# Optimization experiments

Measured on AMD Instinct MI355X. Metric: run time of the kernel, lower is better.

## Reference

```python
import jax, jax.numpy as jnp
import numpy as np

B, T, C, K = 16, 4096, 64, 1024  # K = codebook rows including pad row 0


def setup_inputs() -> dict:
    key = jax.random.key(0)
    k1, k2, k3 = jax.random.split(key, 3)
    z = jax.random.normal(k1, (B, T, C), dtype=jnp.float32)
    codebook_weight = jax.random.normal(k2, (K, C), dtype=jnp.float32)
    # contiguous valid prefixes of random length (torch loop breaks at first 0)
    lengths = jax.random.randint(k3, (B,), T // 2, T + 1)
    mask = (jnp.arange(T)[None, :] < lengths[:, None]).astype(jnp.float32)[:, :, None]
    return {"z": z, "codebook_weight": codebook_weight, "mask": mask}


def _forward(z, codebook_weight, mask):
    # F.normalize(z, p=2, dim=-1) with eps clamp
    z = z / jnp.clip(jnp.linalg.norm(z, axis=-1, keepdims=True), 1e-12)
    e = jax.lax.stop_gradient(codebook_weight)[1:]  # (K-1, C), detached like torch
    zf = z.reshape(-1, C)                            # (B*T, C)
    # squared euclidean distances: ||z||^2 + ||e||^2 - 2 z e^T
    d = (zf * zf).sum(1, keepdims=True) + (e * e).sum(1)[None, :] - 2.0 * (zf @ e.T)
    idx = jnp.argmin(d, axis=1).reshape(B, T)        # (B, T) codes in [0, K-2]
    # scatter(one-hot) @ e  ==  gather rows of e
    z_q = e[idx] * mask                              # (B, T, C)

    valid_count = mask.sum()
    commitment_loss = (jnp.square(z - jax.lax.stop_gradient(z_q)) * mask).sum() / valid_count

    # straight-through estimator
    z_q = z + z_q - jax.lax.stop_gradient(z)

    m1 = mask[:, 1:, :]
    smoothness_loss = (jnp.square(z_q[:, :-1, :] - z_q[:, 1:, :]) * m1).sum() / m1.sum()

    # --- parallel RLE (replaces the host-side python loop) ---
    # torch loop breaks at first mask==0 -> only contiguous valid prefix matters
    mvalid = jnp.cumprod(mask[..., 0], axis=1) > 0   # (B, T) bool
    change = idx[:, 1:] != idx[:, :-1]
    # position 0 always starts a segment; new segment where code changes inside valid prefix
    is_start = jnp.concatenate(
        [jnp.ones((B, 1), dtype=bool), change & mvalid[:, 1:]], axis=1)  # (B, T)
    # stable argsort puts start positions first, in increasing time order
    order = jnp.argsort(jnp.where(is_start, 0, 1), axis=1)               # (B, T)
    n = is_start.sum(axis=1)                                             # segments per batch
    sel_mask = jnp.arange(T)[None, :] < n[:, None]                        # (B, T)
    sel_pos = jnp.where(sel_mask, order, 0)                               # padded to T
    n_mask = sel_mask.astype(jnp.float32)[..., None]                      # (B, T, 1)
    n_z_q = jnp.take_along_axis(z_q, sel_pos[:, :, None], axis=1) * n_mask
    selected_encodings = jnp.where(
        sel_mask, jnp.take_along_axis(idx, sel_pos, axis=1) + 1, 0)       # (B, T) int
    return smoothness_loss, commitment_loss, z_q, n_z_q, n_mask, selected_encodings


def reference(z, codebook_weight, mask):
    return _forward(z, codebook_weight, mask)
```

## Files before the change

### kernel.cpp

```cpp
#include <hip/hip_runtime.h>
#include <math.h>

typedef __attribute__((ext_vector_type(8))) short short8;
typedef __attribute__((ext_vector_type(4))) float f32x4;

#define B_  16
#define T_  4096
#define C_  64
#define KE_ 1023
#define BT_ (B_ * T_)
#define WINHALF 5e-4f


__device__ __forceinline__ unsigned short f2bf(float x) {
    unsigned int u = __float_as_uint(x);
    unsigned int r = (u + 0x7FFFu + ((u >> 16) & 1u)) >> 16;
    return (unsigned short)r;
}
__device__ __forceinline__ float bf2f(unsigned short h) {
    return __uint_as_float(((unsigned int)h) << 16);
}

typedef __attribute__((address_space(1))) const unsigned int g_u32;
typedef __attribute__((address_space(3))) unsigned int l_u32;
__device__ __forceinline__ void gload16(const void* g, void* l) {
    __builtin_amdgcn_global_load_lds((g_u32*)g, (l_u32*)l, 16, 0, 0);
}

__global__ __launch_bounds__(64) void k_prep(const float* __restrict__ cb,
                                             float* __restrict__ ee,
                                             float* __restrict__ ee2,
                                             unsigned short* __restrict__ Eh,
                                             unsigned short* __restrict__ El,
                                             int* __restrict__ flagcnt) {
    const int k = blockIdx.x * 64 + threadIdx.x;
    if (k == 0) *flagcnt = 0;
    unsigned int* EhU = (unsigned int*)Eh;
    unsigned int* ElU = (unsigned int*)El;
    if (k < KE_) {
        const float* r = cb + (size_t)(k + 1) * C_;
        float s = 0.f;
        #pragma unroll
        for (int c = 0; c < C_; c += 2) {
            const float x0 = r[c], x1 = r[c + 1];
            s = fmaf(x0, x0, s);
            s = fmaf(x1, x1, s);
            const float n0 = -x0, n1 = -x1;
            const unsigned short h0 = f2bf(n0), h1 = f2bf(n1);
            const unsigned short l0 = f2bf(n0 - bf2f(h0));
            const unsigned short l1 = f2bf(n1 - bf2f(h1));
            EhU[k * 32 + c / 2] = (unsigned int)h0 | ((unsigned int)h1 << 16);
            ElU[k * 32 + c / 2] = (unsigned int)l0 | ((unsigned int)l1 << 16);
        }
        ee[k]  = s;
        ee2[k] = 0.5f + 0.5f * s;
    } else {
        #pragma unroll
        for (int c = 0; c < 32; ++c) { EhU[k * 32 + c] = 0u; ElU[k * 32 + c] = 0u; }
        ee[k]  = INFINITY;
        ee2[k] = INFINITY;
    }
}

__global__ __launch_bounds__(256, 2) void k_assign(
    const float* __restrict__ z, const unsigned short* __restrict__ Eh,
    const unsigned short* __restrict__ El, const float* __restrict__ ee2,
    int* __restrict__ kbest, int* __restrict__ flaglist,
    int* __restrict__ flagcnt) {

    __shared__ __align__(16) unsigned short s_eh[2][128 * 64];
    __shared__ __align__(16) unsigned short s_el[2][128 * 64];
    __shared__ float s_ee[2][128];

    const int tid  = threadIdx.x;
    const int wave = tid >> 6;
    const int lane = tid & 63;
    const int col  = lane & 15;
    const int quad = lane >> 4;
    const int Q0   = blockIdx.x * 128 + wave * 32;

    short8 ah[2][2], al[2][2];
    #pragma unroll
    for (int g = 0; g < 2; ++g) {
        const float4* zp = (const float4*)(z + (size_t)(Q0 + g * 16 + col) * C_);
        const float4 f0 = zp[quad * 2];
        const float4 f1 = zp[quad * 2 + 1];
        const float4 f2 = zp[8 + quad * 2];
        const float4 f3 = zp[8 + quad * 2 + 1];
        float xs[16] = {f0.x, f0.y, f0.z, f0.w, f1.x, f1.y, f1.z, f1.w,
                        f2.x, f2.y, f2.z, f2.w, f3.x, f3.y, f3.z, f3.w};
        float ss = 0.f;
        #pragma unroll
        for (int i = 0; i < 16; ++i) ss = fmaf(xs[i], xs[i], ss);
        ss += __shfl_xor(ss, 16);
        ss += __shfl_xor(ss, 32);
        const float inv = 1.f / fmaxf(sqrtf(ss), 1e-12f);
        short8 h0, h1, l0, l1;
        #pragma unroll
        for (int i = 0; i < 8; ++i) {
            const float x = xs[i] * inv;
            const unsigned short hx = f2bf(x);
            h0[i] = (short)hx;
            l0[i] = (short)f2bf(x - bf2f(hx));
            const float y = xs[8 + i] * inv;
            const unsigned short hy = f2bf(y);
            h1[i] = (short)hy;
            l1[i] = (short)f2bf(y - bf2f(hy));
        }
        ah[g][0] = h0; ah[g][1] = h1;
        al[g][0] = l0; al[g][1] = l1;
    }

    float bestv[2][4], secv[2][4];
    int   bkk[2][4];
    #pragma unroll
    for (int g = 0; g < 2; ++g)
        #pragma unroll
        for (int r = 0; r < 4; ++r) {
            bestv[g][r] = INFINITY; secv[g][r] = INFINITY; bkk[g][r] = 0;
        }

    const int srow = tid >> 3;
    const int schk = (tid & 7) ^ (srow & 7);
    const int ldsb = (wave * 8) * 64;

#define STAGE_J(tt, bb, j) do {                                                \
        const size_t go = (size_t)((tt) * 128 + (j) * 32 + srow) * 64          \
                          + (size_t)schk * 8;                                  \
        gload16(Eh + go, (void*)&s_eh[bb][ldsb + (j) * 2048]);                 \
        gload16(El + go, (void*)&s_el[bb][ldsb + (j) * 2048]);                 \
    } while (0)

    int cur = 0;
    #pragma unroll
    for (int j = 0; j < 4; ++j) STAGE_J(0, 0, j);
    if (tid < 128) s_ee[0][tid] = ee2[tid];
    __syncthreads();

    const int coff = (quad ^ (col & 7)) * 8;

    for (int t = 0; t < 8; ++t) {
        if (t < 7) { STAGE_J(t + 1, cur ^ 1, 0); STAGE_J(t + 1, cur ^ 1, 1); }

        float ev[8];
        #pragma unroll
        for (int s = 0; s < 8; ++s) ev[s] = s_ee[cur][s * 16 + col];

        short8 fh0 = *(const short8*)&s_eh[cur][col * 64 + coff];
        short8 fh1 = *(const short8*)&s_eh[cur][col * 64 + (coff ^ 32)];
        short8 fl0 = *(const short8*)&s_el[cur][col * 64 + coff];
        short8 fl1 = *(const short8*)&s_el[cur][col * 64 + (coff ^ 32)];

        if (t < 7) {
            STAGE_J(t + 1, cur ^ 1, 2); STAGE_J(t + 1, cur ^ 1, 3);
            if (tid < 128) s_ee[cur ^ 1][tid] = ee2[(t + 1) * 128 + tid];
        }

        const int kb = t * 128 + col;

        #pragma unroll
        for (int s = 0; s < 8; ++s) {
            const int sn = (s < 7) ? (s + 1) : 7;
            const int rb = (sn * 16 + col) * 64;
            short8 nh0 = *(const short8*)&s_eh[cur][rb + coff];
            short8 nh1 = *(const short8*)&s_eh[cur][rb + (coff ^ 32)];
            short8 nl0 = *(const short8*)&s_el[cur][rb + coff];
            short8 nl1 = *(const short8*)&s_el[cur][rb + (coff ^ 32)];

            const float e2 = ev[s];
            f32x4 p0 = {e2, e2, e2, e2};
            f32x4 p1 = {e2, e2, e2, e2};
            __builtin_amdgcn_s_setprio(1);
            p0 = __builtin_amdgcn_mfma_f32_16x16x32_bf16(ah[0][0], fh0, p0, 0, 0, 0);
            p1 = __builtin_amdgcn_mfma_f32_16x16x32_bf16(ah[1][0], fh0, p1, 0, 0, 0);
            p0 = __builtin_amdgcn_mfma_f32_16x16x32_bf16(ah[0][1], fh1, p0, 0, 0, 0);
            p1 = __builtin_amdgcn_mfma_f32_16x16x32_bf16(ah[1][1], fh1, p1, 0, 0, 0);
            p0 = __builtin_amdgcn_mfma_f32_16x16x32_bf16(ah[0][0], fl0, p0, 0, 0, 0);
            p1 = __builtin_amdgcn_mfma_f32_16x16x32_bf16(ah[1][0], fl0, p1, 0, 0, 0);
            p0 = __builtin_amdgcn_mfma_f32_16x16x32_bf16(ah[0][1], fl1, p0, 0, 0, 0);
            p1 = __builtin_amdgcn_mfma_f32_16x16x32_bf16(ah[1][1], fl1, p1, 0, 0, 0);
            p0 = __builtin_amdgcn_mfma_f32_16x16x32_bf16(al[0][0], fh0, p0, 0, 0, 0);
            p1 = __builtin_amdgcn_mfma_f32_16x16x32_bf16(al[1][0], fh0, p1, 0, 0, 0);
            p0 = __builtin_amdgcn_mfma_f32_16x16x32_bf16(al[0][1], fh1, p0, 0, 0, 0);
            p1 = __builtin_amdgcn_mfma_f32_16x16x32_bf16(al[1][1], fh1, p1, 0, 0, 0);
            __builtin_amdgcn_s_setprio(0);

            const int kc = kb + s * 16;
            #pragma unroll
            for (int r = 0; r < 4; ++r) {
                {
                    const float v  = p0[r];
                    const float bo = bestv[0][r];
                    bkk[0][r]   = (v < bo) ? kc : bkk[0][r];
                    secv[0][r]  = fminf(secv[0][r], fmaxf(bo, v));
                    bestv[0][r] = fminf(bo, v);
                }
                {
                    const float v  = p1[r];
                    const float bo = bestv[1][r];
                    bkk[1][r]   = (v < bo) ? kc : bkk[1][r];
                    secv[1][r]  = fminf(secv[1][r], fmaxf(bo, v));
                    bestv[1][r] = fminf(bo, v);
                }
            }
            fh0 = nh0; fh1 = nh1; fl0 = nl0; fl1 = nl1;
        }
        __syncthreads();
        cur ^= 1;
    }
#undef STAGE_J

    #pragma unroll
    for (int g = 0; g < 2; ++g) {
        #pragma unroll
        for (int r = 0; r < 4; ++r) {
            float b  = bestv[g][r], sc = secv[g][r];
            int   k  = bkk[g][r];
            #pragma unroll
            for (int off = 1; off < 16; off <<= 1) {
                const float ob = __shfl_xor(b, off);
                const int   ok = __shfl_xor(k, off);
                const float os = __shfl_xor(sc, off);
                const bool take = (ob < b) || (ob == b && ok < k);
                const float lose = take ? b : ob;
                sc = fminf(fminf(sc, os), lose);
                b  = take ? ob : b;
                k  = take ? ok : k;
            }
            if (col == 0) {
                const int q = Q0 + g * 16 + quad * 4 + r;
                kbest[q] = k;
                if (!(sc - b > WINHALF)) {
                    const int pos = atomicAdd(flagcnt, 1);
                    flaglist[pos] = q;
                }
            }
        }
    }
}

__global__ __launch_bounds__(256) void k_fix(const float* __restrict__ z,
                                             const float* __restrict__ cb,
                                             const float* __restrict__ ee,
                                             const int* __restrict__ flagcnt,
                                             const int* __restrict__ flaglist,
                                             int* __restrict__ kbest) {
    __shared__ float s_z[64];
    __shared__ float s_bv[4];
    __shared__ int   s_bk[4];
    const int tid  = threadIdx.x;
    const int lane = tid & 63;
    const int wave = tid >> 6;
    const int n = *flagcnt;

    for (int i = blockIdx.x; i < n; i += 1024) {
        const int q = flaglist[i];
        __syncthreads();
        if (tid < 16) ((float4*)s_z)[tid] = ((const float4*)(z + (size_t)q * C_))[tid];
        __syncthreads();

        float4 zn[16];
        float ss = 0.f;
        #pragma unroll
        for (int c4 = 0; c4 < 16; ++c4) {
            const float4 v = ((const float4*)s_z)[c4];
            zn[c4] = v;
            ss = fmaf(v.x, v.x, ss); ss = fmaf(v.y, v.y, ss);
            ss = fmaf(v.z, v.z, ss); ss = fmaf(v.w, v.w, ss);
        }
        const float nrm = fmaxf(sqrtf(ss), 1e-12f);
        #pragma unroll
        for (int c4 = 0; c4 < 16; ++c4) {
            zn[c4].x /= nrm; zn[c4].y /= nrm; zn[c4].z /= nrm; zn[c4].w /= nrm;
        }

        const int k0 = tid * 4;
        const float4* e0 = (const float4*)(cb + (size_t)(k0 + 1) * C_);
        const float4* e1 = (const float4*)(cb + (size_t)(k0 + 2) * C_);
        const float4* e2 = (const float4*)(cb + (size_t)(k0 + 3) * C_);
        const float4* e3 = (const float4*)(cb + (size_t)((k0 + 4 <= KE_) ? (k0 + 4) : KE_) * C_);
        float d0 = 0.f, d1 = 0.f, d2 = 0.f, d3 = 0.f;
        #pragma unroll
        for (int c4 = 0; c4 < 16; ++c4) {
            const float4 x = zn[c4];
            const float4 a = e0[c4], b = e1[c4], c = e2[c4], d = e3[c4];
            d0 = fmaf(x.x, a.x, d0); d0 = fmaf(x.y, a.y, d0);
            d0 = fmaf(x.z, a.z, d0); d0 = fmaf(x.w, a.w, d0);
            d1 = fmaf(x.x, b.x, d1); d1 = fmaf(x.y, b.y, d1);
            d1 = fmaf(x.z, b.z, d1); d1 = fmaf(x.w, b.w, d1);
            d2 = fmaf(x.x, c.x, d2); d2 = fmaf(x.y, c.y, d2);
            d2 = fmaf(x.z, c.z, d2); d2 = fmaf(x.w, c.w, d2);
            d3 = fmaf(x.x, d.x, d3); d3 = fmaf(x.y, d.y, d3);
            d3 = fmaf(x.z, d.z, d3); d3 = fmaf(x.w, d.w, d3);
        }
        float bv = INFINITY;
        int   bk = 0;
        float v;
        v = fmaf(-2.f, d0, ee[k0 + 0]); if (v < bv) { bv = v; bk = k0 + 0; }
        v = fmaf(-2.f, d1, ee[k0 + 1]); if (v < bv) { bv = v; bk = k0 + 1; }
        v = fmaf(-2.f, d2, ee[k0 + 2]); if (v < bv) { bv = v; bk = k0 + 2; }
        v = fmaf(-2.f, d3, ee[k0 + 3]); if (v < bv) { bv = v; bk = k0 + 3; }

        #pragma unroll
        for (int off = 32; off > 0; off >>= 1) {
            const float ov = __shfl_down(bv, off);
            const int   ok = __shfl_down(bk, off);
            if (ov < bv || (ov == bv && ok < bk)) { bv = ov; bk = ok; }
        }
        if (lane == 0) { s_bv[wave] = bv; s_bk[wave] = bk; }
        __syncthreads();
        if (tid == 0) {
            float fb = s_bv[0]; int fk = s_bk[0];
            #pragma unroll
            for (int w = 1; w < 4; ++w) {
                if (s_bv[w] < fb || (s_bv[w] == fb && s_bk[w] < fk)) {
                    fb = s_bv[w]; fk = s_bk[w];
                }
            }
            kbest[q] = fk;
        }
    }
}

__global__ __launch_bounds__(256) void k_episcan(
    const float* __restrict__ z, const float* __restrict__ cb,
    const float* __restrict__ mask, const int* __restrict__ kbest,
    float* __restrict__ zqo,
    float* __restrict__ commit_part, float* __restrict__ valid_part,
    float* __restrict__ smooth_part,
    int* __restrict__ selpos, int* __restrict__ nst) {

    const int tid = threadIdx.x;

    if (blockIdx.x < 16) {
        __shared__ int cnt[256];
        const int b = blockIdx.x;
        const int base = b * T_;
        const int t0 = tid * 16;

        int flags = 0, c = 0;
        int prev = (tid == 0) ? -1 : kbest[base + t0 - 1];
        #pragma unroll
        for (int i = 0; i < 16; ++i) {
            const int t = t0 + i;
            const int cur = kbest[base + t];
            const int is = (t == 0) ? 1
                         : ((cur != prev && mask[base + t] > 0.f) ? 1 : 0);
            flags |= is << i;
            c += is;
            prev = cur;
        }
        cnt[tid] = c;
        __syncthreads();
        for (int off = 1; off < 256; off <<= 1) {
            int add = (tid >= off) ? cnt[tid - off] : 0;
            __syncthreads();
            cnt[tid] += add;
            __syncthreads();
        }
        int pos = cnt[tid] - c;
        #pragma unroll
        for (int i = 0; i < 16; ++i) {
            if ((flags >> i) & 1) selpos[base + pos++] = t0 + i;
        }
        if (tid == 255) nst[b] = cnt[255];
        return;
    }

    __shared__ float s_red[12];
    const int bid  = blockIdx.x - 16;
    const int lane = tid & 63;
    const int wave = tid >> 6;
    const int gt   = bid * 256 + tid;
    const int q    = gt >> 2;
    const int p    = gt & 3;
    const int grp  = lane >> 2;

    const int bi = kbest[q];
    const float m = mask[q];

    const float4* zp = (const float4*)(z + (size_t)q * C_ + p * 16);
    const float4* er = (const float4*)(cb + (size_t)(bi + 1) * C_ + p * 16);
    float4* zo = (float4*)(zqo + (size_t)q * C_ + p * 16);

    float4 zr[4];
    float ss = 0.f;
    #pragma unroll
    for (int i = 0; i < 4; ++i) {
        float4 v = zp[i];
        zr[i] = v;
        ss = fmaf(v.x, v.x, ss); ss = fmaf(v.y, v.y, ss);
        ss = fmaf(v.z, v.z, ss); ss = fmaf(v.w, v.w, ss);
    }
    ss += __shfl_xor(ss, 1);
    ss += __shfl_xor(ss, 2);
    const float nrm = fmaxf(sqrtf(ss), 1e-12f);

    float commit = 0.f, sm = 0.f;
    float4 ov[4];
    #pragma unroll
    for (int c4 = 0; c4 < 4; ++c4) {
        const float z0 = zr[c4].x / nrm, z1 = zr[c4].y / nrm;
        const float z2 = zr[c4].z / nrm, z3 = zr[c4].w / nrm;
        const float4 e4 = er[c4];
        const float q0 = e4.x * m, q1 = e4.y * m, q2 = e4.z * m, q3 = e4.w * m;
        float4 o;
        o.x = (z0 + q0) - z0;
        o.y = (z1 + q1) - z1;
        o.z = (z2 + q2) - z2;
        o.w = (z3 + q3) - z3;
        zo[c4] = o;
        ov[c4] = o;
        const float d0 = z0 - q0, d1 = z1 - q1, d2 = z2 - q2, d3 = z3 - q3;
        commit = fmaf(d0, d0, commit); commit = fmaf(d1, d1, commit);
        commit = fmaf(d2, d2, commit); commit = fmaf(d3, d3, commit);
    }
    commit *= m;

    float mnext = 0.f;
    if (grp != 15) mnext = mask[q + 1];
    #pragma unroll
    for (int c4 = 0; c4 < 4; ++c4) {
        const float n0 = __shfl_down(ov[c4].x, 4);
        const float n1 = __shfl_down(ov[c4].y, 4);
        const float n2 = __shfl_down(ov[c4].z, 4);
        const float n3 = __shfl_down(ov[c4].w, 4);
        const float x0 = ov[c4].x - n0, x1 = ov[c4].y - n1;
        const float x2 = ov[c4].z - n2, x3 = ov[c4].w - n3;
        sm = fmaf(x0, x0, sm); sm = fmaf(x1, x1, sm);
        sm = fmaf(x2, x2, sm); sm = fmaf(x3, x3, sm);
    }
    sm *= mnext;

    if (grp == 15) {
        float mn = 0.f;
        if ((q & (T_ - 1)) != T_ - 1) mn = mask[q + 1];
        if (mn > 0.f) {
            const int bi2 = kbest[q + 1];
            const float4* zp2 = (const float4*)(z + (size_t)(q + 1) * C_ + p * 16);
            const float4* er2 = (const float4*)(cb + (size_t)(bi2 + 1) * C_ + p * 16);
            float4 zr2[4];
            float s2 = 0.f;
            #pragma unroll
            for (int i = 0; i < 4; ++i) {
                float4 v = zp2[i];
                zr2[i] = v;
                s2 = fmaf(v.x, v.x, s2); s2 = fmaf(v.y, v.y, s2);
                s2 = fmaf(v.z, v.z, s2); s2 = fmaf(v.w, v.w, s2);
            }
            s2 += __shfl_xor(s2, 1);
            s2 += __shfl_xor(s2, 2);
            const float nrm2 = fmaxf(sqrtf(s2), 1e-12f);
            float smb = 0.f;
            #pragma unroll
            for (int c4 = 0; c4 < 4; ++c4) {
                const float w0 = zr2[c4].x / nrm2, w1 = zr2[c4].y / nrm2;
                const float w2 = zr2[c4].z / nrm2, w3 = zr2[c4].w / nrm2;
                const float4 e4 = er2[c4];
                const float a0 = e4.x * mn, a1 = e4.y * mn;
                const float a2 = e4.z * mn, a3 = e4.w * mn;
                const float o0 = (w0 + a0) - w0;
                const float o1 = (w1 + a1) - w1;
                const float o2 = (w2 + a2) - w2;
                const float o3 = (w3 + a3) - w3;
                const float x0 = ov[c4].x - o0, x1 = ov[c4].y - o1;
                const float x2 = ov[c4].z - o2, x3 = ov[c4].w - o3;
                smb = fmaf(x0, x0, smb); smb = fmaf(x1, x1, smb);
                smb = fmaf(x2, x2, smb); smb = fmaf(x3, x3, smb);
            }
            sm = smb * mn;
        }
    }

    float vc = (p == 0) ? m : 0.f;
    #pragma unroll
    for (int off = 32; off > 0; off >>= 1) {
        commit += __shfl_down(commit, off);
        vc     += __shfl_down(vc, off);
        sm     += __shfl_down(sm, off);
    }
    if (lane == 0) { s_red[wave] = commit; s_red[4 + wave] = vc; s_red[8 + wave] = sm; }
    __syncthreads();
    if (tid == 0) {
        commit_part[bid] = s_red[0] + s_red[1] + s_red[2] + s_red[3];
        valid_part[bid]  = s_red[4] + s_red[5] + s_red[6] + s_red[7];
        smooth_part[bid] = s_red[8] + s_red[9] + s_red[10] + s_red[11];
    }
}

__global__ __launch_bounds__(256) void k_gsel(const float* __restrict__ zqo,
                                              const int* __restrict__ kbest,
                                              const int* __restrict__ selpos,
                                              const int* __restrict__ nst,
                                              const float* __restrict__ commit_part,
                                              const float* __restrict__ valid_part,
                                              const float* __restrict__ smooth_part,
                                              float* __restrict__ nzq,
                                              float* __restrict__ nmask,
                                              float* __restrict__ sel,
                                              float* __restrict__ out) {
    const int gid = blockIdx.x * 256 + threadIdx.x;
    const int b   = gid >> 16;
    const int rem = gid & 65535;
    const int j   = rem >> 4;
    const int c4  = rem & 15;
    const int n   = nst[b];
    float4 v = make_float4(0.f, 0.f, 0.f, 0.f);
    int p = 0;
    if (j < n) {
        p = selpos[b * T_ + j];
        v = ((const float4*)zqo)[((size_t)b * T_ + p) * 16 + c4];
    }
    ((float4*)nzq)[gid] = v;
    if (c4 == 0) {
        float nm = 0.f, s = 0.f;
        if (j < n) { nm = 1.f; s = (float)(kbest[b * T_ + p] + 1); }
        nmask[b * T_ + j] = nm;
        sel[b * T_ + j]   = s;
    }

    if (blockIdx.x == 0) {
        __shared__ double rc[256];
        __shared__ double rv[256];
        __shared__ double rs[256];
        const int tid = threadIdx.x;
        double sc = 0.0, sv = 0.0, ssm = 0.0;
        #pragma unroll
        for (int i = 0; i < 4; ++i) {
            sc  += (double)commit_part[tid + 256 * i];
            sv  += (double)valid_part[tid + 256 * i];
            ssm += (double)smooth_part[tid + 256 * i];
        }
        rc[tid] = sc; rv[tid] = sv; rs[tid] = ssm;
        __syncthreads();
        for (int off = 128; off > 0; off >>= 1) {
            if (tid < off) {
                rc[tid] += rc[tid + off];
                rv[tid] += rv[tid + off];
                rs[tid] += rs[tid + off];
            }
            __syncthreads();
        }
        if (tid == 0) {
            double valid = rv[0];
            out[0] = (float)(rs[0] / (valid - (double)B_));
            out[1] = (float)(rc[0] / valid);
        }
    }
}

extern "C" void kernel_launch(void* const* d_in, const int* in_sizes, int n_in,
                              void* d_out, int out_size, void* d_ws, size_t ws_size,
                              hipStream_t stream) {
    const float* z    = (const float*)d_in[0];
    const float* cb   = (const float*)d_in[1];
    const float* mask = (const float*)d_in[2];
    float* out = (float*)d_out;
    char* ws = (char*)d_ws;

    int*            flagcnt     = (int*)(ws + 0);
    float*          ee          = (float*)(ws + 64);
    unsigned short* Eh          = (unsigned short*)(ws + 4224);
    unsigned short* El          = (unsigned short*)(ws + 135296);
    int*            kbest       = (int*)(ws + 266368);
    int*            selpos      = (int*)(ws + 528512);
    int*            nst         = (int*)(ws + 790656);
    float*          commit_part = (float*)(ws + 791680);
    float*          valid_part  = (float*)(ws + 795776);
    float*          smooth_part = (float*)(ws + 799872);
    int*            flaglist    = (int*)(ws + 804032);
    float*          ee2         = (float*)(ws + 1066176);

    float* zqo   = out + 2;
    float* nzq   = zqo + (size_t)BT_ * C_;
    float* nmask = nzq + (size_t)BT_ * C_;
    float* sel   = nmask + BT_;

    k_prep   <<<16,   64,  0, stream>>>(cb, ee, ee2, Eh, El, flagcnt);
    k_assign <<<512,  256, 0, stream>>>(z, Eh, El, ee2, kbest, flaglist, flagcnt);
    k_fix    <<<1024, 256, 0, stream>>>(z, cb, ee, flagcnt, flaglist, kbest);
    k_episcan<<<1040, 256, 0, stream>>>(z, cb, mask, kbest, zqo,
                                        commit_part, valid_part, smooth_part,
                                        selpos, nst);
    k_gsel   <<<4096, 256, 0, stream>>>(zqo, kbest, selpos, nst,
                                        commit_part, valid_part, smooth_part,
                                        nzq, nmask, sel, out);
}
```

Measured before the change: 139.5 us.

## Parallelize codebook prep per column pair and split MFMA accumulator chains

k_prep now assigns one thread to each pair of codebook columns (128x256 threads) instead of one thread per row, so the bf16 hi/lo split and stores are spread across many more threads, while one thread per row still computes the squared norm. In k_assign the six chained MFMAs per output tile are divided across two independent accumulators that are summed afterwards, which shortens the dependent MFMA chain and lets instructions interleave. The split changes the floating-point summation order and adds a vector add per element, which could shift near-tie argmin decisions slightly and uses more registers.

```diff
diff --git a/kernel.cpp b/kernel.cpp
--- a/kernel.cpp
+++ b/kernel.cpp
@@ -27,38 +27,43 @@
     __builtin_amdgcn_global_load_lds((g_u32*)g, (l_u32*)l, 16, 0, 0);
 }
 
-__global__ __launch_bounds__(64) void k_prep(const float* __restrict__ cb,
-                                             float* __restrict__ ee,
-                                             float* __restrict__ ee2,
-                                             unsigned short* __restrict__ Eh,
-                                             unsigned short* __restrict__ El,
-                                             int* __restrict__ flagcnt) {
-    const int k = blockIdx.x * 64 + threadIdx.x;
-    if (k == 0) *flagcnt = 0;
+__global__ __launch_bounds__(256) void k_prep(const float* __restrict__ cb,
+                                              float* __restrict__ ee,
+                                              float* __restrict__ ee2,
+                                              unsigned short* __restrict__ Eh,
+                                              unsigned short* __restrict__ El,
+                                              int* __restrict__ flagcnt) {
+    const int gid = blockIdx.x * 256 + threadIdx.x;
+    const int k = gid >> 5;
+    const int c = gid & 31;
+    if (gid == 0) *flagcnt = 0;
     unsigned int* EhU = (unsigned int*)Eh;
     unsigned int* ElU = (unsigned int*)El;
     if (k < KE_) {
-        const float* r = cb + (size_t)(k + 1) * C_;
-        float s = 0.f;
-        #pragma unroll
-        for (int c = 0; c < C_; c += 2) {
-            const float x0 = r[c], x1 = r[c + 1];
-            s = fmaf(x0, x0, s);
-            s = fmaf(x1, x1, s);
-            const float n0 = -x0, n1 = -x1;
-            const unsigned short h0 = f2bf(n0), h1 = f2bf(n1);
-            const unsigned short l0 = f2bf(n0 - bf2f(h0));
-            const unsigned short l1 = f2bf(n1 - bf2f(h1));
-            EhU[k * 32 + c / 2] = (unsigned int)h0 | ((unsigned int)h1 << 16);
-            ElU[k * 32 + c / 2] = (unsigned int)l0 | ((unsigned int)l1 << 16);
-        }
-        ee[k]  = s;
-        ee2[k] = 0.5f + 0.5f * s;
+        const float x0 = cb[(size_t)(k + 1) * C_ + 2 * c];
+        const float x1 = cb[(size_t)(k + 1) * C_ + 2 * c + 1];
+        const float n0 = -x0, n1 = -x1;
+        const unsigned short h0 = f2bf(n0), h1 = f2bf(n1);
+        const unsigned short l0 = f2bf(n0 - bf2f(h0));
+        const unsigned short l1 = f2bf(n1 - bf2f(h1));
+        EhU[k * 32 + c] = (unsigned int)h0 | ((unsigned int)h1 << 16);
+        ElU[k * 32 + c] = (unsigned int)l0 | ((unsigned int)l1 << 16);
+        if (c == 0) {
+            const float* r = cb + (size_t)(k + 1) * C_;
+            float s = 0.f;
+            #pragma unroll
+            for (int cc = 0; cc < C_; cc += 2) {
+                const float y0 = r[cc], y1 = r[cc + 1];
+                s = fmaf(y0, y0, s);
+                s = fmaf(y1, y1, s);
+            }
+            ee[k]  = s;
+            ee2[k] = 0.5f + 0.5f * s;
+        }
     } else {
-        #pragma unroll
-        for (int c = 0; c < 32; ++c) { EhU[k * 32 + c] = 0u; ElU[k * 32 + c] = 0u; }
-        ee[k]  = INFINITY;
-        ee2[k] = INFINITY;
+        EhU[k * 32 + c] = 0u;
+        ElU[k * 32 + c] = 0u;
+        if (c == 0) { ee[k] = INFINITY; ee2[k] = INFINITY; }
     }
 }
 
@@ -168,35 +173,35 @@
             short8 nl1 = *(const short8*)&s_el[cur][rb + (coff ^ 32)];
 
             const float e2 = ev[s];
-            f32x4 p0 = {e2, e2, e2, e2};
-            f32x4 p1 = {e2, e2, e2, e2};
+            f32x4 p0a = {e2, e2, e2, e2}, p0b = {0.f, 0.f, 0.f, 0.f};
+            f32x4 p1a = {e2, e2, e2, e2}, p1b = {0.f, 0.f, 0.f, 0.f};
             __builtin_amdgcn_s_setprio(1);
-            p0 = __builtin_amdgcn_mfma_f32_16x16x32_bf16(ah[0][0], fh0, p0, 0, 0, 0);
-            p1 = __builtin_amdgcn_mfma_f32_16x16x32_bf16(ah[1][0], fh0, p1, 0, 0, 0);
-            p0 = __builtin_amdgcn_mfma_f32_16x16x32_bf16(ah[0][1], fh1, p0, 0, 0, 0);
-            p1 = __builtin_amdgcn_mfma_f32_16x16x32_bf16(ah[1][1], fh1, p1, 0, 0, 0);
-            p0 = __builtin_amdgcn_mfma_f32_16x16x32_bf16(ah[0][0], fl0, p0, 0, 0, 0);
-            p1 = __builtin_amdgcn_mfma_f32_16x16x32_bf16(ah[1][0], fl0, p1, 0, 0, 0);
-            p0 = __builtin_amdgcn_mfma_f32_16x16x32_bf16(ah[0][1], fl1, p0, 0, 0, 0);
-            p1 = __builtin_amdgcn_mfma_f32_16x16x32_bf16(ah[1][1], fl1, p1, 0, 0, 0);
-            p0 = __builtin_amdgcn_mfma_f32_16x16x32_bf16(al[0][0], fh0, p0, 0, 0, 0);
-            p1 = __builtin_amdgcn_mfma_f32_16x16x32_bf16(al[1][0], fh0, p1, 0, 0, 0);
-            p0 = __builtin_amdgcn_mfma_f32_16x16x32_bf16(al[0][1], fh1, p0, 0, 0, 0);
-            p1 = __builtin_amdgcn_mfma_f32_16x16x32_bf16(al[1][1], fh1, p1, 0, 0, 0);
+            p0a = __builtin_amdgcn_mfma_f32_16x16x32_bf16(ah[0][0], fh0, p0a, 0, 0, 0);
+            p1a = __builtin_amdgcn_mfma_f32_16x16x32_bf16(ah[1][0], fh0, p1a, 0, 0, 0);
+            p0b = __builtin_amdgcn_mfma_f32_16x16x32_bf16(ah[0][1], fl1, p0b, 0, 0, 0);
+            p1b = __builtin_amdgcn_mfma_f32_16x16x32_bf16(ah[1][1], fl1, p1b, 0, 0, 0);
+            p0a = __builtin_amdgcn_mfma_f32_16x16x32_bf16(ah[0][1], fh1, p0a, 0, 0, 0);
+            p1a = __builtin_amdgcn_mfma_f32_16x16x32_bf16(ah[1][1], fh1, p1a, 0, 0, 0);
+            p0b = __builtin_amdgcn_mfma_f32_16x16x32_bf16(al[0][0], fh0, p0b, 0, 0, 0);
+            p1b = __builtin_amdgcn_mfma_f32_16x16x32_bf16(al[1][0], fh0, p1b, 0, 0, 0);
+            p0a = __builtin_amdgcn_mfma_f32_16x16x32_bf16(ah[0][0], fl0, p0a, 0, 0, 0);
+            p1a = __builtin_amdgcn_mfma_f32_16x16x32_bf16(ah[1][0], fl0, p1a, 0, 0, 0);
+            p0b = __builtin_amdgcn_mfma_f32_16x16x32_bf16(al[0][1], fh1, p0b, 0, 0, 0);
+            p1b = __builtin_amdgcn_mfma_f32_16x16x32_bf16(al[1][1], fh1, p1b, 0, 0, 0);
             __builtin_amdgcn_s_setprio(0);
 
             const int kc = kb + s * 16;
             #pragma unroll
             for (int r = 0; r < 4; ++r) {
                 {
-                    const float v  = p0[r];
+                    const float v  = p0a[r] + p0b[r];
                     const float bo = bestv[0][r];
                     bkk[0][r]   = (v < bo) ? kc : bkk[0][r];
                     secv[0][r]  = fminf(secv[0][r], fmaxf(bo, v));
                     bestv[0][r] = fminf(bo, v);
                 }
                 {
-                    const float v  = p1[r];
+                    const float v  = p1a[r] + p1b[r];
                     const float bo = bestv[1][r];
                     bkk[1][r]   = (v < bo) ? kc : bkk[1][r];
                     secv[1][r]  = fminf(secv[1][r], fmaxf(bo, v));
@@ -576,7 +581,7 @@
     float* nmask = nzq + (size_t)BT_ * C_;
     float* sel   = nmask + BT_;
 
-    k_prep   <<<16,   64,  0, stream>>>(cb, ee, ee2, Eh, El, flagcnt);
+    k_prep   <<<128,  256, 0, stream>>>(cb, ee, ee2, Eh, El, flagcnt);
     k_assign <<<512,  256, 0, stream>>>(z, Eh, El, ee2, kbest, flaglist, flagcnt);
     k_fix    <<<1024, 256, 0, stream>>>(z, cb, ee, flagcnt, flaglist, kbest);
     k_episcan<<<1040, 256, 0, stream>>>(z, cb, mask, kbest, zqo,
```

After: 139.5 us (median of 2 runs). Within noise of the previous version (-0.0%).
